# Performance work log

Hardware: AMD Instinct MI355X
Metric: run time of the kernel (lower is better)

Reference implementation:

```python
import jax, jax.numpy as jnp
import numpy as np

B, I, HID, H, KS = 64, 1024, 2048, 8, 4
D = HID // H  # head_size = 256; also BlockDiagonal block size = (2*I)//H = 256
EPS = 1e-5


def setup_inputs() -> dict:
    key = jax.random.key(0)
    ks = jax.random.split(key, 16)
    r = lambda i, shape, s=0.02: jax.random.normal(ks[i], shape, dtype=jnp.float32) * s
    z = lambda shape: jnp.zeros(shape, jnp.float32)
    return {
        "x": jax.random.normal(ks[0], (B, I), dtype=jnp.float32),
        "h_prev": z((B, H, D)),
        "c_prev": z((B, H, D, D)),
        "n_prev": z((B, H, D)),
        "m_prev": z((B, H)),
        "ln_w": jnp.ones((I,), jnp.float32), "ln_b": z((I,)),
        "W_ul": r(1, (I, HID)), "b_ul": z((HID,)),
        "W_ur": r(2, (I, HID)), "b_ur": z((HID,)),
        "W_conv": r(3, (HID, HID, KS)), "b_conv": z((HID,)),
        "W_skip": r(4, (HID, HID)), "b_skip": z((HID,)),
        "W_q": r(5, (H, D, D)), "b_q": z((HID,)),
        "W_k": r(6, (H, D, D)), "b_k": z((HID,)),
        "W_v": r(7, (H, D, D)), "b_v": z((HID,)),
        "W_i": r(8, (HID, H)), "b_i": z((H,)),
        "W_f": r(9, (HID, H)), "b_f": z((H,)),
        "W_o": r(10, (HID, HID)), "b_o": z((HID,)),
        "W_down": r(11, (HID, I)), "b_down": z((I,)),
        "gn_w": jnp.ones((HID,), jnp.float32), "gn_b": z((HID,)),
    }


def _block_diag(zf, W, b):
    # BlockDiagonal: chunk last dim into H blocks, per-block Linear, concat -> [B,H,D]
    zh = zf.reshape(zf.shape[0], H, -1)
    return jnp.einsum('bhi,hio->bho', zh, W) + b.reshape(H, -1)


def reference(x, h_prev, c_prev, n_prev, m_prev, ln_w, ln_b, W_ul, b_ul, W_ur, b_ur,
              W_conv, b_conv, W_skip, b_skip, W_q, b_q, W_k, b_k, W_v, b_v,
              W_i, b_i, W_f, b_f, W_o, b_o, W_down, b_down, gn_w, gn_b):
    # LayerNorm
    mu = x.mean(-1, keepdims=True)
    var = jnp.mean((x - mu) ** 2, -1, keepdims=True)
    xn = (x - mu) * jax.lax.rsqrt(var + EPS) * ln_w + ln_b
    # Up projections
    xl = xn @ W_ul + b_ul            # [B, 2I] == [B, HID]
    xr = xn @ W_ur + b_ur
    # Causal conv over a length-1 sequence: after left padding + slicing, only the
    # last kernel tap (index KS-1) touches real data -> linear map with W_conv[:,:,KS-1]
    xc = jax.nn.silu(xl @ W_conv[:, :, KS - 1].T + b_conv)
    x_skip = xc @ W_skip + b_skip    # [B, HID]
    q = _block_diag(xc, W_q, b_q)                       # [B,H,D]
    k = _block_diag(xc, W_k, b_k) / jnp.sqrt(jnp.float32(D))
    v = _block_diag(xl, W_v, b_v)
    i_t = xc @ W_i + b_i             # [B,H]
    f_t = xc @ W_f + b_f
    o = jax.nn.sigmoid(xl @ W_o + b_o).reshape(-1, H, D)
    # Stabilized exponential gating
    m_t = jnp.maximum(f_t + m_prev, i_t)
    i_g = jnp.exp(i_t - m_t)
    f_g = jnp.exp(f_t + m_prev - m_t)
    # Outer-product state update + bilinear readout
    c_t = f_g[..., None, None] * c_prev + i_g[..., None, None] * jnp.einsum('bhd,bhk->bhdk', v, k)
    n_t = f_g[..., None] * n_prev + i_g[..., None] * k
    num = jnp.einsum('bhdk,bhk->bhd', c_t, q)
    den = jnp.clip(jnp.einsum('bhd,bhd->bh', n_t, q), 1.0, None)[..., None]
    h_t = o * num / den              # [B,H,D]
    # GroupNorm with num_groups == num_heads: normalize per head
    g_mu = h_t.mean(-1, keepdims=True)
    g_var = jnp.mean((h_t - g_mu) ** 2, -1, keepdims=True)
    gn = ((h_t - g_mu) * jax.lax.rsqrt(g_var + EPS)).reshape(-1, HID) * gn_w + gn_b
    out = (gn + x_skip) * jax.nn.silu(xr)
    out = out @ W_down + b_down
    final = out + x
    return (final, h_t, c_t, n_t, m_t)
```

## Files before the change

kernel.cpp:

```cpp
#include <hip/hip_runtime.h>
#include <cstddef>

typedef __bf16 bf16;
typedef __bf16 bf16x8 __attribute__((ext_vector_type(8)));
typedef short  s16x8  __attribute__((ext_vector_type(8)));
typedef float  f32x4  __attribute__((ext_vector_type(4)));

template <class T> T&& declv() noexcept;
template <class, class = void> struct takes_bf16vec { static constexpr bool value = false; };
template <class V> struct takes_bf16vec<V, decltype((void)__builtin_amdgcn_mfma_f32_16x16x32_bf16(
    declv<V>(), declv<V>(), declv<f32x4>(), 0, 0, 0))> { static constexpr bool value = true; };

template <class V>
__device__ __forceinline__ f32x4 mfma_bf16_16x16x32(V a, V b, f32x4 c) {
  if constexpr (takes_bf16vec<V>::value) {
    return __builtin_amdgcn_mfma_f32_16x16x32_bf16(a, b, c, 0, 0, 0);
  } else {
    return __builtin_amdgcn_mfma_f32_16x16x32_bf16(
        __builtin_bit_cast(s16x8, a), __builtin_bit_cast(s16x8, b), c, 0, 0, 0);
  }
}

constexpr int M_NONE = 0, M_SILU = 1, M_SIG = 2, M_SCALE = 3, M_FINAL = 4;

__global__ __launch_bounds__(256) void ln_kernel(const float* __restrict__ x,
                                                 const float* __restrict__ w,
                                                 const float* __restrict__ bs,
                                                 bf16* __restrict__ xn) {
  const int b = blockIdx.x, tid = threadIdx.x;
  __shared__ float red[256];
  float vals[4];
  float s = 0.f;
#pragma unroll
  for (int i = 0; i < 4; ++i) { vals[i] = x[b * 1024 + i * 256 + tid]; s += vals[i]; }
  red[tid] = s; __syncthreads();
  for (int off = 128; off; off >>= 1) { if (tid < off) red[tid] += red[tid + off]; __syncthreads(); }
  const float mu = red[0] * (1.f / 1024.f);
  __syncthreads();
  float s2 = 0.f;
#pragma unroll
  for (int i = 0; i < 4; ++i) { const float d = vals[i] - mu; s2 += d * d; }
  red[tid] = s2; __syncthreads();
  for (int off = 128; off; off >>= 1) { if (tid < off) red[tid] += red[tid + off]; __syncthreads(); }
  const float rs = rsqrtf(red[0] * (1.f / 1024.f) + 1e-5f);
#pragma unroll
  for (int i = 0; i < 4; ++i) {
    const int j = i * 256 + tid;
    xn[b * 1024 + j] = (bf16)((vals[i] - mu) * rs * w[j] + bs[j]);
  }
}

template <int K, int KS, int NTILES, bool S4, bool DUAL>
__global__ __launch_bounds__(256) void gemm_part(
    const bf16* __restrict__ A0, const bf16* __restrict__ A1,
    const float* __restrict__ W0, const float* __restrict__ W1,
    int ldA, int ldB, float* __restrict__ part) {
  constexpr int Ncomb = NTILES * 16;
  constexpr int Kslice = K / KS;
  constexpr int chunk = Kslice / 4;
  const int tid = threadIdx.x;
  const int lane = tid & 63, wave = tid >> 6;
  const int l15 = lane & 15, quad = lane >> 4;
  const int tile = blockIdx.x % NTILES, ks = blockIdx.x / NTILES;

  const bf16* A = A0;
  const float* W = W0;
  int ncol;
  if (DUAL) {
    const int seg = tile >> 7;
    if (seg) { A = A1; W = W1; }
    ncol = (tile & 127) * 16;
  } else {
    ncol = tile * 16;
  }
  const int kbeg = ks * Kslice + wave * chunk;

  f32x4 acc0{}, acc1{}, acc2{}, acc3{};
#pragma unroll
  for (int k = 0; k < chunk; k += 32) {
    const int kk = kbeg + k + quad * 8;
    bf16x8 bfrag;
    if (S4) {
      const float* wp = W + ((size_t)(ncol + l15) * 2048 + kk) * 4 + 3;
#pragma unroll
      for (int j = 0; j < 8; ++j) bfrag[j] = (bf16)wp[j * 4];
    } else {
      const float* wp = W + (size_t)kk * ldB + ncol + l15;
#pragma unroll
      for (int j = 0; j < 8; ++j) bfrag[j] = (bf16)wp[(size_t)j * ldB];
    }
    const bf16* ap = A + (size_t)l15 * ldA + kk;
    const size_t st = (size_t)16 * ldA;
    bf16x8 a0 = *(const bf16x8*)(ap);
    bf16x8 a1 = *(const bf16x8*)(ap + st);
    bf16x8 a2 = *(const bf16x8*)(ap + 2 * st);
    bf16x8 a3 = *(const bf16x8*)(ap + 3 * st);
    acc0 = mfma_bf16_16x16x32(a0, bfrag, acc0);
    acc1 = mfma_bf16_16x16x32(a1, bfrag, acc1);
    acc2 = mfma_bf16_16x16x32(a2, bfrag, acc2);
    acc3 = mfma_bf16_16x16x32(a3, bfrag, acc3);
  }
  __shared__ float lds[4][64][20];
#pragma unroll
  for (int r = 0; r < 4; ++r) {
    const int rr = quad * 4 + r;
    lds[wave][rr][l15]      = acc0[r];
    lds[wave][16 + rr][l15] = acc1[r];
    lds[wave][32 + rr][l15] = acc2[r];
    lds[wave][48 + rr][l15] = acc3[r];
  }
  __syncthreads();
  const int col = tid & 15, rb = (tid >> 4) << 2;
#pragma unroll
  for (int r2 = 0; r2 < 4; ++r2) {
    const int row = rb + r2;
    const float v = lds[0][row][col] + lds[1][row][col] + lds[2][row][col] + lds[3][row][col];
    part[((size_t)ks * 64 + row) * Ncomb + tile * 16 + col] = v;
  }
}

__global__ __launch_bounds__(256) void combine(
    const float* __restrict__ part, int KS, int Ncomb, int halfN,
    const float* __restrict__ bias0, const float* __restrict__ bias1,
    int mode0, int mode1,
    float* __restrict__ outF0, bf16* __restrict__ outB0,
    float* __restrict__ outF1, bf16* __restrict__ outB1,
    const float* __restrict__ xadd) {
  const int e = (blockIdx.x * 256 + threadIdx.x) * 4;
  const int total = 64 * Ncomb;
  if (e >= total) return;
  const int row = e / Ncomb, col = e - row * Ncomb;
  float4 s = *(const float4*)(part + e);
  for (int ks = 1; ks < KS; ++ks) {
    const float4 p = *(const float4*)(part + (size_t)ks * total + e);
    s.x += p.x; s.y += p.y; s.z += p.z; s.w += p.w;
  }
  const int seg = (col >= halfN) ? 1 : 0;
  const int cn = col - seg * halfN;
  const float* bias = seg ? bias1 : bias0;
  const int mode = seg ? mode1 : mode0;
  float* outF = seg ? outF1 : outF0;
  bf16* outB = seg ? outB1 : outB0;
  float vv[4] = {s.x, s.y, s.z, s.w};
#pragma unroll
  for (int j = 0; j < 4; ++j) {
    float v = vv[j] + bias[cn + j];
    if (mode == M_SILU)       v = v / (1.f + expf(-v));
    else if (mode == M_SIG)   v = 1.f / (1.f + expf(-v));
    else if (mode == M_SCALE) v *= 0.0625f;
    else if (mode == M_FINAL) v += xadd[(size_t)row * halfN + cn + j];
    const size_t oi = (size_t)row * halfN + cn + j;
    if (outF) outF[oi] = v;
    if (outB) outB[oi] = (bf16)v;
  }
}

__global__ __launch_bounds__(256) void gemm_qkv(
    const bf16* __restrict__ xc, const bf16* __restrict__ xl,
    const float* __restrict__ Wq, const float* __restrict__ bq,
    const float* __restrict__ Wk, const float* __restrict__ bk,
    const float* __restrict__ Wv, const float* __restrict__ bv,
    float* __restrict__ qf, float* __restrict__ kf, float* __restrict__ vf) {
  const int tid = threadIdx.x;
  const int lane = tid & 63, wave = tid >> 6;
  const int l15 = lane & 15, quad = lane >> 4;
  const int seg = blockIdx.x >> 7, t = blockIdx.x & 127;
  const int n0 = t * 16, h = t >> 4, wn0 = n0 & 255;
  const bf16* A = (seg == 2) ? xl : xc;
  const float* W = (seg == 0) ? Wq : (seg == 1) ? Wk : Wv;
  const float* bias = (seg == 0) ? bq : (seg == 1) ? bk : bv;
  float* out = (seg == 0) ? qf : (seg == 1) ? kf : vf;
  const float* Wb = W + (size_t)h * 65536;
  const int aCol0 = h << 8;
  const int kbeg = wave * 64;

  f32x4 acc0{}, acc1{}, acc2{}, acc3{};
#pragma unroll
  for (int k = 0; k < 64; k += 32) {
    const int kk = kbeg + k + quad * 8;
    bf16x8 bfrag;
    const float* wp = Wb + (size_t)kk * 256 + wn0 + l15;
#pragma unroll
    for (int j = 0; j < 8; ++j) bfrag[j] = (bf16)wp[(size_t)j * 256];
    const bf16* ap = A + (size_t)l15 * 2048 + aCol0 + kk;
    const size_t st = (size_t)16 * 2048;
    bf16x8 a0 = *(const bf16x8*)(ap);
    bf16x8 a1 = *(const bf16x8*)(ap + st);
    bf16x8 a2 = *(const bf16x8*)(ap + 2 * st);
    bf16x8 a3 = *(const bf16x8*)(ap + 3 * st);
    acc0 = mfma_bf16_16x16x32(a0, bfrag, acc0);
    acc1 = mfma_bf16_16x16x32(a1, bfrag, acc1);
    acc2 = mfma_bf16_16x16x32(a2, bfrag, acc2);
    acc3 = mfma_bf16_16x16x32(a3, bfrag, acc3);
  }
  __shared__ float lds[4][64][20];
#pragma unroll
  for (int r = 0; r < 4; ++r) {
    const int rr = quad * 4 + r;
    lds[wave][rr][l15]      = acc0[r];
    lds[wave][16 + rr][l15] = acc1[r];
    lds[wave][32 + rr][l15] = acc2[r];
    lds[wave][48 + rr][l15] = acc3[r];
  }
  __syncthreads();
  const int col = tid & 15, rb = (tid >> 4) << 2;
  const float bv_ = bias[n0 + col];
#pragma unroll
  for (int r2 = 0; r2 < 4; ++r2) {
    const int row = rb + r2;
    float v = lds[0][row][col] + lds[1][row][col] + lds[2][row][col] + lds[3][row][col] + bv_;
    if (seg == 1) v *= 0.0625f;
    out[(size_t)row * 2048 + n0 + col] = v;
  }
}

__global__ __launch_bounds__(256) void gemm_sk(
    const bf16* __restrict__ A, const float* __restrict__ W,
    const float* __restrict__ bias, const float* __restrict__ xadd,
    float* __restrict__ outF, bf16* __restrict__ outB,
    int K, int N, int ldA, int mode) {
  const int tid = threadIdx.x;
  const int lane = tid & 63, wave = tid >> 6;
  const int l15 = lane & 15, quad = lane >> 4;
  const int n0 = blockIdx.x << 4;
  const int ldB = N;
  const int kchunk = K >> 2;
  const int kbeg = wave * kchunk, kend = kbeg + kchunk;

  f32x4 acc0{}, acc1{}, acc2{}, acc3{};
  for (int k = kbeg; k < kend; k += 32) {
    const int kk = k + quad * 8;
    bf16x8 bfrag;
    const float* wp = W + (size_t)kk * ldB + n0 + l15;
#pragma unroll
    for (int j = 0; j < 8; ++j) bfrag[j] = (bf16)wp[(size_t)j * ldB];
    const bf16* ap = A + (size_t)l15 * ldA + kk;
    const size_t st = (size_t)16 * ldA;
    bf16x8 a0 = *(const bf16x8*)(ap);
    bf16x8 a1 = *(const bf16x8*)(ap + st);
    bf16x8 a2 = *(const bf16x8*)(ap + 2 * st);
    bf16x8 a3 = *(const bf16x8*)(ap + 3 * st);
    acc0 = mfma_bf16_16x16x32(a0, bfrag, acc0);
    acc1 = mfma_bf16_16x16x32(a1, bfrag, acc1);
    acc2 = mfma_bf16_16x16x32(a2, bfrag, acc2);
    acc3 = mfma_bf16_16x16x32(a3, bfrag, acc3);
  }
  __shared__ float lds[4][64][20];
#pragma unroll
  for (int r = 0; r < 4; ++r) {
    const int rr = quad * 4 + r;
    lds[wave][rr][l15]      = acc0[r];
    lds[wave][16 + rr][l15] = acc1[r];
    lds[wave][32 + rr][l15] = acc2[r];
    lds[wave][48 + rr][l15] = acc3[r];
  }
  __syncthreads();
  const int col = tid & 15, rb = (tid >> 4) << 2;
  const float bv = bias[n0 + col];
#pragma unroll
  for (int r2 = 0; r2 < 4; ++r2) {
    const int row = rb + r2;
    float v = lds[0][row][col] + lds[1][row][col] + lds[2][row][col] + lds[3][row][col] + bv;
    if (mode == M_FINAL) v += xadd[(size_t)row * N + n0 + col];
    const size_t oi = (size_t)row * N + n0 + col;
    if (outF) outF[oi] = v;
    if (outB) outB[oi] = (bf16)v;
  }
}

__global__ __launch_bounds__(256) void gates_kernel(
    const bf16* __restrict__ xc, const float* __restrict__ Wi, const float* __restrict__ bi,
    const float* __restrict__ Wf, const float* __restrict__ bfv, const float* __restrict__ m_prev,
    float* __restrict__ ig, float* __restrict__ fg, float* __restrict__ mt_out) {
  const int b = blockIdx.x, tid = threadIdx.x;
  float ai[8] = {}, af[8] = {};
  for (int k = tid; k < 2048; k += 256) {
    const float xv = (float)xc[b * 2048 + k];
    const float4 wi0 = *(const float4*)(Wi + (size_t)k * 8);
    const float4 wi1 = *(const float4*)(Wi + (size_t)k * 8 + 4);
    const float4 wf0 = *(const float4*)(Wf + (size_t)k * 8);
    const float4 wf1 = *(const float4*)(Wf + (size_t)k * 8 + 4);
    ai[0] += xv * wi0.x; ai[1] += xv * wi0.y; ai[2] += xv * wi0.z; ai[3] += xv * wi0.w;
    ai[4] += xv * wi1.x; ai[5] += xv * wi1.y; ai[6] += xv * wi1.z; ai[7] += xv * wi1.w;
    af[0] += xv * wf0.x; af[1] += xv * wf0.y; af[2] += xv * wf0.z; af[3] += xv * wf0.w;
    af[4] += xv * wf1.x; af[5] += xv * wf1.y; af[6] += xv * wf1.z; af[7] += xv * wf1.w;
  }
  __shared__ float ri[256][8], rf[256][8];
#pragma unroll
  for (int h = 0; h < 8; ++h) { ri[tid][h] = ai[h]; rf[tid][h] = af[h]; }
  __syncthreads();
  for (int off = 128; off; off >>= 1) {
    if (tid < off) {
#pragma unroll
      for (int h = 0; h < 8; ++h) { ri[tid][h] += ri[tid + off][h]; rf[tid][h] += rf[tid + off][h]; }
    }
    __syncthreads();
  }
  if (tid < 8) {
    const float it = ri[0][tid] + bi[tid];
    const float ft = rf[0][tid] + bfv[tid];
    const float mp = m_prev[b * 8 + tid];
    const float mt = fmaxf(ft + mp, it);
    mt_out[b * 8 + tid] = mt;
    ig[b * 8 + tid] = expf(it - mt);
    fg[b * 8 + tid] = expf(ft + mp - mt);
  }
}

__global__ __launch_bounds__(256) void state1(
    const float* __restrict__ c_prev, const float* __restrict__ qf,
    const float* __restrict__ kf, const float* __restrict__ vf,
    const float* __restrict__ ig, const float* __restrict__ fg,
    float* __restrict__ ct_out, float* __restrict__ numw) {
  const int bh = blockIdx.x >> 3, rg = blockIdx.x & 7;
  const int tid = threadIdx.x;
  const int b = bh >> 3, h = bh & 7, vb = b * 2048 + h * 256;
  __shared__ float q_s[256], k_s[256];
  q_s[tid] = qf[vb + tid];
  k_s[tid] = kf[vb + tid];
  __syncthreads();
  const float i_g = ig[bh], f_g = fg[bh];
  const int row = rg * 32 + (tid >> 3);
  const int lane8 = tid & 7;
  const float vd = vf[vb + row];
  const float iv = i_g * vd;
  const size_t base = ((size_t)bh << 16) + ((size_t)row << 8) + lane8 * 4;
  float p = 0.f;
#pragma unroll
  for (int i = 0; i < 8; ++i) {
    const int c = lane8 * 4 + i * 32;
    const float4 cp = *(const float4*)(c_prev + base + i * 32);
    float4 cn;
    cn.x = f_g * cp.x + iv * k_s[c];
    cn.y = f_g * cp.y + iv * k_s[c + 1];
    cn.z = f_g * cp.z + iv * k_s[c + 2];
    cn.w = f_g * cp.w + iv * k_s[c + 3];
    *(float4*)(ct_out + base + i * 32) = cn;
    p += cn.x * q_s[c] + cn.y * q_s[c + 1] + cn.z * q_s[c + 2] + cn.w * q_s[c + 3];
  }
#pragma unroll
  for (int m = 1; m < 8; m <<= 1) p += __shfl_xor(p, m, 64);
  if (lane8 == 0) numw[bh * 256 + row] = p;
}

__global__ __launch_bounds__(256) void state2(
    const float* __restrict__ n_prev, const float* __restrict__ qf,
    const float* __restrict__ kf, const float* __restrict__ of,
    const float* __restrict__ ig, const float* __restrict__ fg,
    const float* numw, const float* __restrict__ xskip,
    const float* __restrict__ xrf, const float* __restrict__ gnw,
    const float* __restrict__ gnb, float* __restrict__ nt_out,
    float* ht_out, bf16* __restrict__ pre_bf) {
  const int bh = blockIdx.x, b = bh >> 3, h = bh & 7;
  const int tid = threadIdx.x;
  const int vb = b * 2048 + h * 256;
  __shared__ float red[256];
  const float i_g = ig[bh], f_g = fg[bh];
  const float qv = qf[vb + tid], kv = kf[vb + tid];
  const float nv = f_g * n_prev[bh * 256 + tid] + i_g * kv;
  nt_out[bh * 256 + tid] = nv;
  red[tid] = nv * qv;
  __syncthreads();
  for (int off = 128; off; off >>= 1) { if (tid < off) red[tid] += red[tid + off]; __syncthreads(); }
  const float den = fmaxf(red[0], 1.0f);
  const float num = numw[bh * 256 + tid];
  const float hv = of[vb + tid] * num / den;
  ht_out[bh * 256 + tid] = hv;
  __syncthreads();
  red[tid] = hv; __syncthreads();
  for (int off = 128; off; off >>= 1) { if (tid < off) red[tid] += red[tid + off]; __syncthreads(); }
  const float mu = red[0] * (1.f / 256.f);
  __syncthreads();
  const float dv = hv - mu;
  red[tid] = dv * dv; __syncthreads();
  for (int off = 128; off; off >>= 1) { if (tid < off) red[tid] += red[tid + off]; __syncthreads(); }
  const float gn = (hv - mu) * rsqrtf(red[0] * (1.f / 256.f) + 1e-5f);
  const int j = h * 256 + tid;
  const float xr = xrf[b * 2048 + j];
  const float pre = (gn * gnw[j] + gnb[j] + xskip[b * 2048 + j]) * (xr / (1.f + expf(-xr)));
  pre_bf[b * 2048 + j] = (bf16)pre;
}

extern "C" void kernel_launch(void* const* d_in, const int* in_sizes, int n_in,
                              void* d_out, int out_size, void* d_ws, size_t ws_size,
                              hipStream_t stream) {
  (void)in_sizes; (void)n_in; (void)out_size; (void)ws_size;
  const float* x      = (const float*)d_in[0];
  const float* c_prev = (const float*)d_in[2];
  const float* n_prev = (const float*)d_in[3];
  const float* m_prev = (const float*)d_in[4];
  const float* ln_w = (const float*)d_in[5];
  const float* ln_b = (const float*)d_in[6];
  const float* W_ul = (const float*)d_in[7];
  const float* b_ul = (const float*)d_in[8];
  const float* W_ur = (const float*)d_in[9];
  const float* b_ur = (const float*)d_in[10];
  const float* W_conv = (const float*)d_in[11];
  const float* b_conv = (const float*)d_in[12];
  const float* W_skip = (const float*)d_in[13];
  const float* b_skip = (const float*)d_in[14];
  const float* W_q = (const float*)d_in[15];
  const float* b_q = (const float*)d_in[16];
  const float* W_k = (const float*)d_in[17];
  const float* b_k = (const float*)d_in[18];
  const float* W_v = (const float*)d_in[19];
  const float* b_v = (const float*)d_in[20];
  const float* W_i = (const float*)d_in[21];
  const float* b_i = (const float*)d_in[22];
  const float* W_f = (const float*)d_in[23];
  const float* b_f = (const float*)d_in[24];
  const float* W_o = (const float*)d_in[25];
  const float* b_o = (const float*)d_in[26];
  const float* W_down = (const float*)d_in[27];
  const float* b_down = (const float*)d_in[28];
  const float* gn_w = (const float*)d_in[29];
  const float* gn_b = (const float*)d_in[30];

  float* out_final = (float*)d_out;
  float* out_ht = out_final + 65536;
  float* out_ct = out_final + 196608;
  float* out_nt = out_final + 33751040;
  float* out_mt = out_final + 33882112;

  char* ws = (char*)d_ws;
  bf16*  xn_bf   = (bf16*)(ws + 0);
  bf16*  xl_bf   = (bf16*)(ws + 131072);
  bf16*  xc_bf   = (bf16*)(ws + 393216);
  bf16*  pre_bf  = (bf16*)(ws + 655360);
  float* xr_f    = (float*)(ws + 917504);
  float* xskip_f = (float*)(ws + 1441792);
  float* q_f     = (float*)(ws + 1966080);
  float* k_f     = (float*)(ws + 2490368);
  float* v_f     = (float*)(ws + 3014656);
  float* o_f     = (float*)(ws + 3538944);
  float* ig_f    = (float*)(ws + 4063232);
  float* fg_f    = (float*)(ws + 4065280);
  float* num_f   = out_ht;
  float* part    = out_ct;

  ln_kernel<<<64, 256, 0, stream>>>(x, ln_w, ln_b, xn_bf);
  gemm_part<1024, 4, 256, false, true><<<1024, 256, 0, stream>>>(
      xn_bf, xn_bf, W_ul, W_ur, 1024, 2048, part);
  combine<<<256, 256, 0, stream>>>(part, 4, 4096, 2048, b_ul, b_ur, M_NONE, M_NONE,
                                   nullptr, xl_bf, xr_f, nullptr, nullptr);
  gemm_part<2048, 8, 128, true, false><<<1024, 256, 0, stream>>>(
      xl_bf, nullptr, W_conv, nullptr, 2048, 2048, part);
  combine<<<128, 256, 0, stream>>>(part, 8, 2048, 2048, b_conv, nullptr, M_SILU, M_NONE,
                                   nullptr, xc_bf, nullptr, nullptr, nullptr);
  gemm_part<2048, 4, 256, false, true><<<1024, 256, 0, stream>>>(
      xc_bf, xl_bf, W_skip, W_o, 2048, 2048, part);
  combine<<<256, 256, 0, stream>>>(part, 4, 4096, 2048, b_skip, b_o, M_NONE, M_SIG,
                                   xskip_f, nullptr, o_f, nullptr, nullptr);
  gemm_qkv<<<384, 256, 0, stream>>>(xc_bf, xl_bf, W_q, b_q, W_k, b_k, W_v, b_v,
                                    q_f, k_f, v_f);
  gates_kernel<<<64, 256, 0, stream>>>(xc_bf, W_i, b_i, W_f, b_f, m_prev, ig_f, fg_f, out_mt);
  state1<<<4096, 256, 0, stream>>>(c_prev, q_f, k_f, v_f, ig_f, fg_f, out_ct, num_f);
  state2<<<512, 256, 0, stream>>>(n_prev, q_f, k_f, o_f, ig_f, fg_f, num_f,
                                  xskip_f, xr_f, gn_w, gn_b, out_nt, out_ht, pre_bf);
  gemm_sk<<<64, 256, 0, stream>>>(pre_bf, W_down, b_down, x, out_final, nullptr,
                                  2048, 1024, 2048, M_FINAL);
}
```

Before: 448.8 us.

## Repack conv weight to bf16 and split-K the down projection with atomics

Adds a repack kernel that extracts the last conv tap into a contiguous bf16 [N,K] matrix, so the conv GEMM loads 16-byte vectors instead of strided fp32 gathers. The repack runs on every call, so it still reads the full 64MB W_conv, but as coalesced float4 loads. Replaces the 64-block down-projection kernel with a 512-block split-K gemm_part that atomically accumulates into the output. The output is pre-seeded in the LayerNorm kernel with x plus b_down. This adds parallelism to the final GEMM, at the cost of atomic traffic and a summation order that is no longer deterministic.

```diff
diff --git a/kernel.cpp b/kernel.cpp
--- a/kernel.cpp
+++ b/kernel.cpp
@@ -21,12 +21,25 @@
   }
 }
 
-constexpr int M_NONE = 0, M_SILU = 1, M_SIG = 2, M_SCALE = 3, M_FINAL = 4;
+constexpr int M_NONE = 0, M_SILU = 1, M_SIG = 2;
+
+__global__ __launch_bounds__(256) void repack_wc(const float* __restrict__ Wc,
+                                                 bf16* __restrict__ Wp) {
+  const int n = blockIdx.x;
+  const float4* src = (const float4*)(Wc + (size_t)n * 8192);
+  bf16* dst = Wp + (size_t)n * 2048;
+  for (int k = threadIdx.x; k < 2048; k += 256) {
+    const float4 t = src[k];
+    dst[k] = (bf16)t.w;
+  }
+}
 
 __global__ __launch_bounds__(256) void ln_kernel(const float* __restrict__ x,
                                                  const float* __restrict__ w,
                                                  const float* __restrict__ bs,
-                                                 bf16* __restrict__ xn) {
+                                                 const float* __restrict__ bdown,
+                                                 bf16* __restrict__ xn,
+                                                 float* __restrict__ outf) {
   const int b = blockIdx.x, tid = threadIdx.x;
   __shared__ float red[256];
   float vals[4];
@@ -47,14 +60,16 @@
   for (int i = 0; i < 4; ++i) {
     const int j = i * 256 + tid;
     xn[b * 1024 + j] = (bf16)((vals[i] - mu) * rs * w[j] + bs[j]);
-  }
-}
-
-template <int K, int KS, int NTILES, bool S4, bool DUAL>
+    outf[b * 1024 + j] = vals[i] + bdown[j];
+  }
+}
+
+template <int K, int KS, int NTILES, bool BT, bool DUAL, bool ATOMIC>
 __global__ __launch_bounds__(256) void gemm_part(
     const bf16* __restrict__ A0, const bf16* __restrict__ A1,
     const float* __restrict__ W0, const float* __restrict__ W1,
-    int ldA, int ldB, float* __restrict__ part) {
+    const bf16* __restrict__ Wb,
+    int ldA, int ldB, float* __restrict__ dst, int outN) {
   constexpr int Ncomb = NTILES * 16;
   constexpr int Kslice = K / KS;
   constexpr int chunk = Kslice / 4;
@@ -80,10 +95,8 @@
   for (int k = 0; k < chunk; k += 32) {
     const int kk = kbeg + k + quad * 8;
     bf16x8 bfrag;
-    if (S4) {
-      const float* wp = W + ((size_t)(ncol + l15) * 2048 + kk) * 4 + 3;
-#pragma unroll
-      for (int j = 0; j < 8; ++j) bfrag[j] = (bf16)wp[j * 4];
+    if (BT) {
+      bfrag = *(const bf16x8*)(Wb + (size_t)(ncol + l15) * K + kk);
     } else {
       const float* wp = W + (size_t)kk * ldB + ncol + l15;
 #pragma unroll
@@ -115,7 +128,11 @@
   for (int r2 = 0; r2 < 4; ++r2) {
     const int row = rb + r2;
     const float v = lds[0][row][col] + lds[1][row][col] + lds[2][row][col] + lds[3][row][col];
-    part[((size_t)ks * 64 + row) * Ncomb + tile * 16 + col] = v;
+    if (ATOMIC) {
+      atomicAdd(dst + (size_t)row * outN + tile * 16 + col, v);
+    } else {
+      dst[((size_t)ks * 64 + row) * Ncomb + tile * 16 + col] = v;
+    }
   }
 }
 
@@ -124,8 +141,7 @@
     const float* __restrict__ bias0, const float* __restrict__ bias1,
     int mode0, int mode1,
     float* __restrict__ outF0, bf16* __restrict__ outB0,
-    float* __restrict__ outF1, bf16* __restrict__ outB1,
-    const float* __restrict__ xadd) {
+    float* __restrict__ outF1, bf16* __restrict__ outB1) {
   const int e = (blockIdx.x * 256 + threadIdx.x) * 4;
   const int total = 64 * Ncomb;
   if (e >= total) return;
@@ -147,8 +163,6 @@
     float v = vv[j] + bias[cn + j];
     if (mode == M_SILU)       v = v / (1.f + expf(-v));
     else if (mode == M_SIG)   v = 1.f / (1.f + expf(-v));
-    else if (mode == M_SCALE) v *= 0.0625f;
-    else if (mode == M_FINAL) v += xadd[(size_t)row * halfN + cn + j];
     const size_t oi = (size_t)row * halfN + cn + j;
     if (outF) outF[oi] = v;
     if (outB) outB[oi] = (bf16)v;
@@ -211,60 +225,6 @@
     float v = lds[0][row][col] + lds[1][row][col] + lds[2][row][col] + lds[3][row][col] + bv_;
     if (seg == 1) v *= 0.0625f;
     out[(size_t)row * 2048 + n0 + col] = v;
-  }
-}
-
-__global__ __launch_bounds__(256) void gemm_sk(
-    const bf16* __restrict__ A, const float* __restrict__ W,
-    const float* __restrict__ bias, const float* __restrict__ xadd,
-    float* __restrict__ outF, bf16* __restrict__ outB,
-    int K, int N, int ldA, int mode) {
-  const int tid = threadIdx.x;
-  const int lane = tid & 63, wave = tid >> 6;
-  const int l15 = lane & 15, quad = lane >> 4;
-  const int n0 = blockIdx.x << 4;
-  const int ldB = N;
-  const int kchunk = K >> 2;
-  const int kbeg = wave * kchunk, kend = kbeg + kchunk;
-
-  f32x4 acc0{}, acc1{}, acc2{}, acc3{};
-  for (int k = kbeg; k < kend; k += 32) {
-    const int kk = k + quad * 8;
-    bf16x8 bfrag;
-    const float* wp = W + (size_t)kk * ldB + n0 + l15;
-#pragma unroll
-    for (int j = 0; j < 8; ++j) bfrag[j] = (bf16)wp[(size_t)j * ldB];
-    const bf16* ap = A + (size_t)l15 * ldA + kk;
-    const size_t st = (size_t)16 * ldA;
-    bf16x8 a0 = *(const bf16x8*)(ap);
-    bf16x8 a1 = *(const bf16x8*)(ap + st);
-    bf16x8 a2 = *(const bf16x8*)(ap + 2 * st);
-    bf16x8 a3 = *(const bf16x8*)(ap + 3 * st);
-    acc0 = mfma_bf16_16x16x32(a0, bfrag, acc0);
-    acc1 = mfma_bf16_16x16x32(a1, bfrag, acc1);
-    acc2 = mfma_bf16_16x16x32(a2, bfrag, acc2);
-    acc3 = mfma_bf16_16x16x32(a3, bfrag, acc3);
-  }
-  __shared__ float lds[4][64][20];
-#pragma unroll
-  for (int r = 0; r < 4; ++r) {
-    const int rr = quad * 4 + r;
-    lds[wave][rr][l15]      = acc0[r];
-    lds[wave][16 + rr][l15] = acc1[r];
-    lds[wave][32 + rr][l15] = acc2[r];
-    lds[wave][48 + rr][l15] = acc3[r];
-  }
-  __syncthreads();
-  const int col = tid & 15, rb = (tid >> 4) << 2;
-  const float bv = bias[n0 + col];
-#pragma unroll
-  for (int r2 = 0; r2 < 4; ++r2) {
-    const int row = rb + r2;
-    float v = lds[0][row][col] + lds[1][row][col] + lds[2][row][col] + lds[3][row][col] + bv;
-    if (mode == M_FINAL) v += xadd[(size_t)row * N + n0 + col];
-    const size_t oi = (size_t)row * N + n0 + col;
-    if (outF) outF[oi] = v;
-    if (outB) outB[oi] = (bf16)v;
   }
 }
 
@@ -435,28 +395,30 @@
   float* o_f     = (float*)(ws + 3538944);
   float* ig_f    = (float*)(ws + 4063232);
   float* fg_f    = (float*)(ws + 4065280);
+  bf16*  wcp     = (bf16*)(ws + 4067328);
   float* num_f   = out_ht;
   float* part    = out_ct;
 
-  ln_kernel<<<64, 256, 0, stream>>>(x, ln_w, ln_b, xn_bf);
-  gemm_part<1024, 4, 256, false, true><<<1024, 256, 0, stream>>>(
-      xn_bf, xn_bf, W_ul, W_ur, 1024, 2048, part);
+  repack_wc<<<2048, 256, 0, stream>>>(W_conv, wcp);
+  ln_kernel<<<64, 256, 0, stream>>>(x, ln_w, ln_b, b_down, xn_bf, out_final);
+  gemm_part<1024, 4, 256, false, true, false><<<1024, 256, 0, stream>>>(
+      xn_bf, xn_bf, W_ul, W_ur, nullptr, 1024, 2048, part, 0);
   combine<<<256, 256, 0, stream>>>(part, 4, 4096, 2048, b_ul, b_ur, M_NONE, M_NONE,
-                                   nullptr, xl_bf, xr_f, nullptr, nullptr);
-  gemm_part<2048, 8, 128, true, false><<<1024, 256, 0, stream>>>(
-      xl_bf, nullptr, W_conv, nullptr, 2048, 2048, part);
+                                   nullptr, xl_bf, xr_f, nullptr);
+  gemm_part<2048, 8, 128, true, false, false><<<1024, 256, 0, stream>>>(
+      xl_bf, nullptr, nullptr, nullptr, wcp, 2048, 2048, part, 0);
   combine<<<128, 256, 0, stream>>>(part, 8, 2048, 2048, b_conv, nullptr, M_SILU, M_NONE,
-                                   nullptr, xc_bf, nullptr, nullptr, nullptr);
-  gemm_part<2048, 4, 256, false, true><<<1024, 256, 0, stream>>>(
-      xc_bf, xl_bf, W_skip, W_o, 2048, 2048, part);
+                                   nullptr, xc_bf, nullptr, nullptr);
+  gemm_part<2048, 4, 256, false, true, false><<<1024, 256, 0, stream>>>(
+      xc_bf, xl_bf, W_skip, W_o, nullptr, 2048, 2048, part, 0);
   combine<<<256, 256, 0, stream>>>(part, 4, 4096, 2048, b_skip, b_o, M_NONE, M_SIG,
-                                   xskip_f, nullptr, o_f, nullptr, nullptr);
+                                   xskip_f, nullptr, o_f, nullptr);
   gemm_qkv<<<384, 256, 0, stream>>>(xc_bf, xl_bf, W_q, b_q, W_k, b_k, W_v, b_v,
                                     q_f, k_f, v_f);
   gates_kernel<<<64, 256, 0, stream>>>(xc_bf, W_i, b_i, W_f, b_f, m_prev, ig_f, fg_f, out_mt);
   state1<<<4096, 256, 0, stream>>>(c_prev, q_f, k_f, v_f, ig_f, fg_f, out_ct, num_f);
   state2<<<512, 256, 0, stream>>>(n_prev, q_f, k_f, o_f, ig_f, fg_f, num_f,
                                   xskip_f, xr_f, gn_w, gn_b, out_nt, out_ht, pre_bf);
-  gemm_sk<<<64, 256, 0, stream>>>(pre_bf, W_down, b_down, x, out_final, nullptr,
-                                  2048, 1024, 2048, M_FINAL);
-}
+  gemm_part<2048, 8, 64, false, false, true><<<512, 256, 0, stream>>>(
+      pre_bf, nullptr, W_down, nullptr, nullptr, 2048, 1024, out_final, 1024);
+}
```

New measurement: 438.0 us. 1.02x faster.
